# Optimization experiments

Measured on AMD Instinct MI355X. Metric: run time of the kernel, lower is better.

The kernel has to match this reference:

```python
import jax, jax.numpy as jnp
import numpy as np

N_NODES = 50000
N_ENT = 100000
N_REL = 200
DE = 100
DR = 100
B = 16
E2 = 600000
U = 500


def setup_inputs() -> dict:
    key = jax.random.key(0)
    ks = jax.random.split(key, 16)
    f32 = jnp.float32
    return {
        "entity_table": jax.random.normal(ks[0], (N_ENT, DE), f32),
        "relation_table": jax.random.normal(ks[1], (N_REL, DR), f32),
        "total_unseen_embedding": jax.random.normal(ks[2], (U, DE), f32),
        "att_mu": jax.random.normal(ks[3], (2 * N_REL, B), f32) * 0.1,
        "basis_mu": jax.random.normal(ks[4], (B, DE + DR, DE), f32) * 0.05,
        "root_mu": jax.random.normal(ks[5], (DE, DE), f32) * 0.1,
        "bias_mu": jnp.zeros((DE,), f32),
        "att_sigma": jax.random.normal(ks[6], (2 * N_REL, B), f32) * 0.1,
        "basis_sigma": jax.random.normal(ks[7], (B, DE + DR, DE), f32) * 0.05,
        "root_sigma": jax.random.normal(ks[8], (DE, DE), f32) * 0.1,
        "bias_sigma": jnp.zeros((DE,), f32),
        "node_id": jax.random.randint(ks[9], (N_NODES,), 0, N_ENT),
        "edge_index": jax.random.randint(ks[10], (2, E2), 0, N_NODES),
        "edge_type": jax.random.randint(ks[11], (E2,), 0, 2 * N_REL),
        "rel_index": jax.random.randint(ks[12], (E2,), 0, N_REL),
        "unseen_index": jax.random.randint(ks[13], (U,), 0, N_NODES),
    }


def gen_conv(m, edge_type, dst, x, att, basis, root, bias, n_nodes):
    """Basis-decomposed relational conv with mean aggregation (GENConv).

    m: [E, in] per-edge concat(x_src, rel_emb); msg_e = m_e @ (att[type_e] @ basis).
    Computed as sum_b coeff[:, b] * (m @ basis[b]) to avoid an [E, in, out] gather.
    """
    coeff = att[edge_type]  # [E, B]
    msg = coeff[:, 0:1] * (m @ basis[0])
    for b in range(1, basis.shape[0]):
        msg = msg + coeff[:, b:b + 1] * (m @ basis[b])
    agg = jax.ops.segment_sum(msg, dst, num_segments=n_nodes)  # [N, out]
    cnt = jax.ops.segment_sum(jnp.ones((m.shape[0],), m.dtype), dst,
                              num_segments=n_nodes)
    agg = agg / jnp.maximum(cnt, 1.0)[:, None]  # scatter-mean, empty nodes -> 0
    return agg + x @ root + bias


def reference(entity_table, relation_table, total_unseen_embedding,
              att_mu, basis_mu, root_mu, bias_mu,
              att_sigma, basis_sigma, root_sigma, bias_sigma,
              node_id, edge_index, edge_type, rel_index, unseen_index):
    x = entity_table[node_id]  # [N, De]
    x = x.at[unseen_index].set(total_unseen_embedding)
    rel_emb = relation_table[rel_index]  # [E, Dr]
    src, dst = edge_index[0], edge_index[1]
    m = jnp.concatenate([x[src], rel_emb], axis=1)  # [E, De+Dr]
    n = x.shape[0]
    mu = gen_conv(m, edge_type, dst, x, att_mu, basis_mu, root_mu, bias_mu, n)
    logvar = gen_conv(m, edge_type, dst, x, att_sigma, basis_sigma,
                      root_sigma, bias_sigma, n)
    # eval mode: reparameterize -> mu, dropout -> identity
    unseen = mu[unseen_index]
    return unseen, mu[unseen_index], logvar[unseen_index]
```

## Files before the change

### kernel.cpp

```cpp
#include <hip/hip_runtime.h>
#include <stdint.h>

#define E2V     600000
#define NNODES  50000
#define UCNT    500
#define DE      100
#define DOUT    100
#define NB      16
#define KTOT    3328
#define MROWS   512
#define HASHN   2048
#define HCAP    64
#define NREG    586
#define ECAP    96
#define TRB     832

using short8 = __attribute__((ext_vector_type(8))) short;
using f32x4  = __attribute__((ext_vector_type(4))) float;

static constexpr size_t align256(size_t x){ return (x + 255) & ~size_t(255); }
static constexpr size_t OFF_HCNT = 0;
static constexpr size_t OFF_IHEA = align256(OFF_HCNT + NREG*4);
static constexpr size_t OFF_INEX = OFF_IHEA + MROWS*4;
static constexpr size_t OFF_HBUF = align256(OFF_INEX + MROWS*4);
static constexpr size_t OFF_GM   = align256(OFF_HBUF + (size_t)NREG*HCAP*8);
static constexpr size_t OFF_GS   = OFF_GM + (size_t)MROWS*KTOT*2;
static constexpr size_t OFF_BTM  = align256(OFF_GS + (size_t)MROWS*KTOT*2);
static constexpr size_t OFF_BTS  = OFF_BTM + (size_t)DOUT*KTOT*2;

__device__ __forceinline__ unsigned short f2b(float f){
    uint32_t u = __float_as_uint(f);
    uint32_t r = (u + 0x7FFFu + ((u >> 16) & 1u)) >> 16;
    return (unsigned short)r;
}

__device__ __forceinline__ uint32_t hh(int key){
    return (((uint32_t)key * 2654435761u) >> 16) & (HASHN - 1);
}
__device__ __forceinline__ void hins(int* hk, int* hv, int key, int val){
    uint32_t idx = hh(key);
    while (true){
        int k = hk[idx];
        if (k == key){ atomicMax(&hv[idx], val); return; }
        if (k == -1){
            int old = atomicCAS(&hk[idx], -1, key);
            if (old == -1 || old == key){ atomicMax(&hv[idx], val); return; }
        }
        idx = (idx + 1) & (HASHN - 1);
    }
}
__device__ __forceinline__ int hlook(const int* hk, const int* hv, int key){
    uint32_t idx = hh(key);
    while (true){
        int k = hk[idx];
        if (k == key) return hv[idx];
        if (k == -1)  return -1;
        idx = (idx + 1) & (HASHN - 1);
    }
}

__device__ __forceinline__ float bt_src(const float* __restrict__ basis,
                                        const float* __restrict__ root,
                                        const float* __restrict__ bias,
                                        int k, int j){
    if (j >= 100) return 0.f;
    if (k < 3200) return basis[k*100 + j];
    if (k < 3300) return root[(k-3200)*100 + j];
    if (k == 3300) return bias[j];
    return 0.f;
}

__global__ __launch_bounds__(256) void k1(
        const int* __restrict__ unseen_index, const int* __restrict__ eidx,
        int* __restrict__ hcnt, uint64_t* __restrict__ hbuf,
        int* __restrict__ ihead, int* __restrict__ inext,
        const float* __restrict__ bm, const float* __restrict__ bs,
        const float* __restrict__ rm, const float* __restrict__ rs,
        const float* __restrict__ qm, const float* __restrict__ qs,
        unsigned short* __restrict__ btm, unsigned short* __restrict__ bts){
    __shared__ int hk[HASHN], hv[HASHN];
    __shared__ float tile[32][33];
    __shared__ uint64_t sHit[HCAP];
    __shared__ int sN, sIH[MROWS];
    int bx = blockIdx.x, tid = threadIdx.x;

    if (bx < NREG){
        for (int i = tid; i < HASHN; i += 256){ hk[i] = -1; hv[i] = -1; }
        if (tid == 0) sN = 0;
        __syncthreads();
        for (int u = tid; u < UCNT; u += 256) hins(hk, hv, unseen_index[u], u);
        __syncthreads();
        int e0 = bx*1024 + tid*4;
        if (e0 < E2V){
            int4 d = *(const int4*)(eidx + E2V + e0);
            #pragma unroll
            for (int j = 0; j < 4; ++j){
                int dn = (j==0) ? d.x : (j==1) ? d.y : (j==2) ? d.z : d.w;
                int s = hlook(hk, hv, dn);
                if (s >= 0){
                    int e = e0 + j;
                    int srcp = hlook(hk, hv, eidx[e]);
                    int p = atomicAdd(&sN, 1);
                    if (p < HCAP)
                        sHit[p] = ((uint64_t)(uint32_t)(srcp + 1) << 32)
                                | ((uint64_t)(uint32_t)s << 20) | (uint64_t)(uint32_t)e;
                }
            }
        }
        __syncthreads();
        int n = sN < HCAP ? sN : HCAP;
        if (tid == 0) hcnt[bx] = n;
        if (tid < n) hbuf[bx*HCAP + tid] = sHit[tid];
        return;
    }
    if (bx < NREG + TRB){
        int b2 = bx - NREG;
        int kt = b2 % 104, jt = (b2 / 104) & 3, br = b2 / 416;
        const float* basis = br ? bs : bm;
        const float* root  = br ? rs : rm;
        const float* bias  = br ? qs : qm;
        unsigned short* bt = br ? bts : btm;
        int k0 = kt*32, j0 = jt*32;
        int tx = tid & 31, ty = tid >> 5;
        for (int r = ty; r < 32; r += 8)
            tile[r][tx] = bt_src(basis, root, bias, k0 + r, j0 + tx);
        __syncthreads();
        for (int r = ty; r < 32; r += 8){
            int j = j0 + r;
            if (j < 100) bt[(size_t)j*KTOT + k0 + tx] = f2b(tile[tx][r]);
        }
        return;
    }
    for (int i = tid; i < HASHN; i += 256){ hk[i] = -1; hv[i] = -1; }
    for (int i = tid; i < MROWS; i += 256) sIH[i] = -1;
    __syncthreads();
    for (int u = tid; u < UCNT; u += 256) hins(hk, hv, unseen_index[u], u);
    __syncthreads();
    for (int u = tid; u < UCNT; u += 256){
        int slot = hlook(hk, hv, unseen_index[u]);
        inext[u] = atomicExch(&sIH[slot], u);
    }
    __syncthreads();
    for (int i = tid; i < MROWS; i += 256) ihead[i] = sIH[i];
}

__global__ __launch_bounds__(256) void k_g(
        const int* __restrict__ hcnt, const uint64_t* __restrict__ hbuf,
        const int* __restrict__ eidx,
        const int* __restrict__ etype, const int* __restrict__ rel_index,
        const int* __restrict__ node_id,
        const float* __restrict__ ent, const float* __restrict__ unseen,
        const float* __restrict__ rel,
        const float* __restrict__ am, const float* __restrict__ as_,
        unsigned short* __restrict__ Gm, unsigned short* __restrict__ Gs){
    int slot = blockIdx.x;
    int tid  = threadIdx.x;
    __shared__ int sEdge[ECAP], sNE;
    __shared__ short sSrc[ECAP];
    __shared__ __align__(16) float sM[8][200];
    __shared__ __align__(16) float sAm[8][16], sAs[8][16];
    __shared__ const float* sPX[8];
    __shared__ const float* sPR[8];
    __shared__ int sT[8];

    if (tid == 0) sNE = 0;
    __syncthreads();
    for (int r = tid; r < NREG; r += 256){
        int c = hcnt[r];
        for (int i = 0; i < c; ++i){
            uint64_t h = hbuf[r*HCAP + i];
            if ((int)((h >> 20) & 0xFFFu) == slot){
                int p = atomicAdd(&sNE, 1);
                if (p < ECAP){
                    sEdge[p] = (int)(h & 0xFFFFFu);
                    sSrc[p]  = (short)((int)(uint32_t)(h >> 32) - 1);
                }
            }
        }
    }
    __syncthreads();
    int nT = sNE;
    int nE = nT > ECAP ? ECAP : nT;

    float gm[16], gs[16];
    #pragma unroll
    for (int b = 0; b < NB; ++b){ gm[b] = 0.f; gs[b] = 0.f; }

    for (int c0 = 0; c0 < nE; c0 += 8){
        int kc = nE - c0; if (kc > 8) kc = 8;
        if (tid < kc){
            int e = sEdge[c0 + tid];
            sT[tid] = etype[e];
            int srcp = sSrc[c0 + tid];
            sPX[tid] = (srcp >= 0) ? unseen + (size_t)srcp*DE
                                   : ent + (size_t)node_id[eidx[e]]*DE;
            sPR[tid] = rel + (size_t)rel_index[e]*DE;
        }
        __syncthreads();
        for (int q = tid; q < kc*50; q += 256){
            int eL = q / 50, s = q % 50;
            const float* base = (s < 25) ? sPX[eL] : sPR[eL];
            int off = (s < 25) ? s*4 : (s-25)*4;
            float4 v = *(const float4*)(base + off);
            int kb = (s < 25) ? s*4 : (s-25)*4 + 100;
            *(float4*)&sM[eL][kb] = v;
        }
        if (tid < kc*16){
            int eL = tid >> 4, b = tid & 15;
            int t = sT[eL];
            sAm[eL][b] = am[t*NB + b];
            sAs[eL][b] = as_[t*NB + b];
        }
        __syncthreads();
        if (tid < 200){
            for (int e = 0; e < kc; ++e){
                float mk = sM[e][tid];
                const float4* pa = (const float4*)&sAm[e][0];
                const float4* ps = (const float4*)&sAs[e][0];
                #pragma unroll
                for (int q = 0; q < 4; ++q){
                    float4 va = pa[q], vs = ps[q];
                    gm[q*4+0] += va.x*mk; gm[q*4+1] += va.y*mk;
                    gm[q*4+2] += va.z*mk; gm[q*4+3] += va.w*mk;
                    gs[q*4+0] += vs.x*mk; gs[q*4+1] += vs.y*mk;
                    gs[q*4+2] += vs.z*mk; gs[q*4+3] += vs.w*mk;
                }
            }
        }
        __syncthreads();
    }
    size_t row = (size_t)slot * KTOT;
    float inv = 1.f / fmaxf((float)nT, 1.f);
    if (tid < 200){
        #pragma unroll
        for (int b = 0; b < NB; ++b){
            Gm[row + b*200 + tid] = f2b(gm[b] * inv);
            Gs[row + b*200 + tid] = f2b(gs[b] * inv);
        }
    }
    if (tid < 100){
        float xv = (slot < UCNT) ? unseen[(size_t)slot*DE + tid] : 0.f;
        unsigned short h = f2b(xv);
        Gm[row + 3200 + tid] = h; Gs[row + 3200 + tid] = h;
    } else if (tid == 100){
        Gm[row + 3300] = f2b(1.f); Gs[row + 3300] = f2b(1.f);
    } else if (tid > 100 && tid < 128){
        Gm[row + 3200 + tid] = 0; Gs[row + 3200 + tid] = 0;
    }
}

__global__ __launch_bounds__(512) void k_gemm(
        const unsigned short* __restrict__ Gm, const unsigned short* __restrict__ Gs,
        const unsigned short* __restrict__ Btm, const unsigned short* __restrict__ Bts,
        const int* __restrict__ ihead, const int* __restrict__ inext,
        float* __restrict__ out){
    __shared__ f32x4 red[512];
    int bid = blockIdx.x;
    int br  = bid / 224;
    int w2  = bid % 224;
    int m16 = w2 & 31;
    int jt  = w2 >> 5;
    int wv  = threadIdx.x >> 6;
    int lane = threadIdx.x & 63;
    const unsigned short* A  = br ? Gs : Gm;
    const unsigned short* Bt = br ? Bts : Btm;
    int rowa = lane & 15, ko = (lane >> 4) * 8;
    int j0 = (jt == 6) ? 84 : jt*16;
    int col = j0 + rowa;
    const unsigned short* ap = A  + (size_t)(m16*16 + rowa)*KTOT + ko + wv*416;
    const unsigned short* bp = Bt + (size_t)col*KTOT + ko + wv*416;
    short8 avs[13], bvs[13];
    #pragma unroll
    for (int kc = 0; kc < 13; ++kc){
        avs[kc] = *(const short8*)(ap + kc*32);
        bvs[kc] = *(const short8*)(bp + kc*32);
    }
    f32x4 acc = {0.f, 0.f, 0.f, 0.f};
    #pragma unroll
    for (int kc = 0; kc < 13; ++kc)
        acc = __builtin_amdgcn_mfma_f32_16x16x32_bf16(avs[kc], bvs[kc], acc, 0, 0, 0);
    red[threadIdx.x] = acc;
    __syncthreads();
    if (threadIdx.x < 64){
        #pragma unroll
        for (int w = 1; w < 8; ++w){
            f32x4 o = red[threadIdx.x + w*64];
            acc[0] += o[0]; acc[1] += o[1]; acc[2] += o[2]; acc[3] += o[3];
        }
        if (jt < 6 || col >= 96){
            int r0 = m16*16 + (lane >> 4)*4;
            #pragma unroll
            for (int r = 0; r < 4; ++r){
                int u = ihead[r0 + r];
                while (u >= 0){
                    if (br == 0){
                        out[(size_t)u*100 + col] = acc[r];
                        out[(size_t)(UCNT + u)*100 + col] = acc[r];
                    } else {
                        out[(size_t)(2*UCNT + u)*100 + col] = acc[r];
                    }
                    u = inext[u];
                }
            }
        }
    }
}

extern "C" void kernel_launch(void* const* d_in, const int* in_sizes, int n_in,
                              void* d_out, int out_size, void* d_ws, size_t ws_size,
                              hipStream_t stream){
    const float* ent        = (const float*)d_in[0];
    const float* rel_table  = (const float*)d_in[1];
    const float* unseen_emb = (const float*)d_in[2];
    const float* att_mu     = (const float*)d_in[3];
    const float* basis_mu   = (const float*)d_in[4];
    const float* root_mu    = (const float*)d_in[5];
    const float* bias_mu    = (const float*)d_in[6];
    const float* att_sig    = (const float*)d_in[7];
    const float* basis_sig  = (const float*)d_in[8];
    const float* root_sig   = (const float*)d_in[9];
    const float* bias_sig   = (const float*)d_in[10];
    const int* node_id      = (const int*)d_in[11];
    const int* edge_index   = (const int*)d_in[12];
    const int* edge_type    = (const int*)d_in[13];
    const int* rel_index    = (const int*)d_in[14];
    const int* unseen_index = (const int*)d_in[15];
    float* out = (float*)d_out;
    char* ws = (char*)d_ws;

    int* hcnt       = (int*)(ws + OFF_HCNT);
    int* ihead      = (int*)(ws + OFF_IHEA);
    int* inext      = (int*)(ws + OFF_INEX);
    uint64_t* hbuf  = (uint64_t*)(ws + OFF_HBUF);
    unsigned short* Gm  = (unsigned short*)(ws + OFF_GM);
    unsigned short* Gs  = (unsigned short*)(ws + OFF_GS);
    unsigned short* Btm = (unsigned short*)(ws + OFF_BTM);
    unsigned short* Bts = (unsigned short*)(ws + OFF_BTS);

    k1<<<NREG + TRB + 1, 256, 0, stream>>>(unseen_index, edge_index,
        hcnt, hbuf, ihead, inext,
        basis_mu, basis_sig, root_mu, root_sig, bias_mu, bias_sig, Btm, Bts);
    k_g<<<MROWS, 256, 0, stream>>>(hcnt, hbuf, edge_index, edge_type,
        rel_index, node_id, ent, unseen_emb, rel_table, att_mu, att_sig, Gm, Gs);
    k_gemm<<<448, 512, 0, stream>>>(Gm, Gs, Btm, Bts, ihead, inext, out);
}
```

Measured before the change: 48.74 us.

## Pre-swizzle A and B operands into MFMA fragment order for coalesced loads

The gather kernel writes the G matrices, and the transpose blocks write the basis matrices, directly in the per-wave MFMA fragment layout. Each lane's 16-byte load in the GEMM then falls in a contiguous 1 KB chunk instead of rows strided by KTOT. B is duplicated per 16-column tile, with the overlapping tile 84-99 stored twice. The cost is scattered 2-byte stores in the producer kernels and a larger B buffer.

```diff
diff --git a/kernel.cpp b/kernel.cpp
--- a/kernel.cpp
+++ b/kernel.cpp
@@ -14,6 +14,7 @@
 #define NREG    586
 #define ECAP    96
 #define TRB     832
+#define BFN     (7*8*13*512)
 
 using short8 = __attribute__((ext_vector_type(8))) short;
 using f32x4  = __attribute__((ext_vector_type(4))) float;
@@ -26,12 +27,19 @@
 static constexpr size_t OFF_GM   = align256(OFF_HBUF + (size_t)NREG*HCAP*8);
 static constexpr size_t OFF_GS   = OFF_GM + (size_t)MROWS*KTOT*2;
 static constexpr size_t OFF_BTM  = align256(OFF_GS + (size_t)MROWS*KTOT*2);
-static constexpr size_t OFF_BTS  = OFF_BTM + (size_t)DOUT*KTOT*2;
+static constexpr size_t OFF_BTS  = OFF_BTM + (size_t)BFN*2;
 
 __device__ __forceinline__ unsigned short f2b(float f){
     uint32_t u = __float_as_uint(f);
     uint32_t r = (u + 0x7FFFu + ((u >> 16) & 1u)) >> 16;
     return (unsigned short)r;
+}
+
+__device__ __forceinline__ size_t af_idx(int row, int k){
+    int mt = row >> 4, lr = row & 15;
+    int wv = k / 416, r = k - wv*416;
+    int kc = r >> 5, hi = (r >> 3) & 3, off = r & 7;
+    return ((size_t)((mt*8 + wv)*13 + kc) << 9) + (size_t)((hi*16 + lr) << 3) + off;
 }
 
 __device__ __forceinline__ uint32_t hh(int key){
@@ -79,7 +87,6 @@
         const float* __restrict__ qm, const float* __restrict__ qs,
         unsigned short* __restrict__ btm, unsigned short* __restrict__ bts){
     __shared__ int hk[HASHN], hv[HASHN];
-    __shared__ float tile[32][33];
     __shared__ uint64_t sHit[HCAP];
     __shared__ int sN, sIH[MROWS];
     int bx = blockIdx.x, tid = threadIdx.x;
@@ -115,19 +122,29 @@
     }
     if (bx < NREG + TRB){
         int b2 = bx - NREG;
-        int kt = b2 % 104, jt = (b2 / 104) & 3, br = b2 / 416;
+        int kt = b2 % 104, jt4 = (b2 / 104) & 3, br = b2 / 416;
         const float* basis = br ? bs : bm;
         const float* root  = br ? rs : rm;
         const float* bias  = br ? qs : qm;
         unsigned short* bt = br ? bts : btm;
-        int k0 = kt*32, j0 = jt*32;
-        int tx = tid & 31, ty = tid >> 5;
-        for (int r = ty; r < 32; r += 8)
-            tile[r][tx] = bt_src(basis, root, bias, k0 + r, j0 + tx);
-        __syncthreads();
-        for (int r = ty; r < 32; r += 8){
-            int j = j0 + r;
-            if (j < 100) bt[(size_t)j*KTOT + k0 + tx] = f2b(tile[tx][r]);
+        int k0 = kt*32, j0t = jt4*32;
+        for (int q = tid; q < 1024; q += 256){
+            int kk = q >> 5, jj = q & 31;
+            int k = k0 + kk, j = j0t + jj;
+            if (j >= 100) continue;
+            unsigned short hv16 = f2b(bt_src(basis, root, bias, k, j));
+            int wv = k / 416, r = k - wv*416;
+            int kc = r >> 5, hi = (r >> 3) & 3, off = r & 7;
+            #pragma unroll
+            for (int t7 = 0; t7 < 7; ++t7){
+                int tj0 = (t7 == 6) ? 84 : t7*16;
+                int lr = j - tj0;
+                if (lr >= 0 && lr < 16){
+                    size_t idx = ((size_t)((t7*8 + wv)*13 + kc) << 9)
+                               + (size_t)((hi*16 + lr) << 3) + off;
+                    bt[idx] = hv16;
+                }
+            }
         }
         return;
     }
@@ -229,23 +246,27 @@
         }
         __syncthreads();
     }
-    size_t row = (size_t)slot * KTOT;
     float inv = 1.f / fmaxf((float)nT, 1.f);
     if (tid < 200){
         #pragma unroll
         for (int b = 0; b < NB; ++b){
-            Gm[row + b*200 + tid] = f2b(gm[b] * inv);
-            Gs[row + b*200 + tid] = f2b(gs[b] * inv);
+            int k = b*200 + tid;
+            size_t ix = af_idx(slot, k);
+            Gm[ix] = f2b(gm[b] * inv);
+            Gs[ix] = f2b(gs[b] * inv);
         }
     }
     if (tid < 100){
         float xv = (slot < UCNT) ? unseen[(size_t)slot*DE + tid] : 0.f;
         unsigned short h = f2b(xv);
-        Gm[row + 3200 + tid] = h; Gs[row + 3200 + tid] = h;
+        size_t ix = af_idx(slot, 3200 + tid);
+        Gm[ix] = h; Gs[ix] = h;
     } else if (tid == 100){
-        Gm[row + 3300] = f2b(1.f); Gs[row + 3300] = f2b(1.f);
+        size_t ix = af_idx(slot, 3300);
+        Gm[ix] = f2b(1.f); Gs[ix] = f2b(1.f);
     } else if (tid > 100 && tid < 128){
-        Gm[row + 3200 + tid] = 0; Gs[row + 3200 + tid] = 0;
+        size_t ix = af_idx(slot, 3200 + tid);
+        Gm[ix] = 0; Gs[ix] = 0;
     }
 }
 
@@ -264,16 +285,16 @@
     int lane = threadIdx.x & 63;
     const unsigned short* A  = br ? Gs : Gm;
     const unsigned short* Bt = br ? Bts : Btm;
-    int rowa = lane & 15, ko = (lane >> 4) * 8;
+    int rowa = lane & 15;
     int j0 = (jt == 6) ? 84 : jt*16;
     int col = j0 + rowa;
-    const unsigned short* ap = A  + (size_t)(m16*16 + rowa)*KTOT + ko + wv*416;
-    const unsigned short* bp = Bt + (size_t)col*KTOT + ko + wv*416;
+    const unsigned short* ap = A  + (((size_t)(m16*8 + wv)*13) << 9) + ((size_t)lane << 3);
+    const unsigned short* bp = Bt + (((size_t)(jt*8 + wv)*13) << 9) + ((size_t)lane << 3);
     short8 avs[13], bvs[13];
     #pragma unroll
     for (int kc = 0; kc < 13; ++kc){
-        avs[kc] = *(const short8*)(ap + kc*32);
-        bvs[kc] = *(const short8*)(bp + kc*32);
+        avs[kc] = *(const short8*)(ap + kc*512);
+        bvs[kc] = *(const short8*)(bp + kc*512);
     }
     f32x4 acc = {0.f, 0.f, 0.f, 0.f};
     #pragma unroll
```

New measurement: 44.38 us, median of 2. -9.0%, faster.
